# Kernel tuning notes

Measured on AMD Instinct MI355X. Metric: run time of the kernel, lower is better.

Reference implementation:

```python
import jax, jax.numpy as jnp
import numpy as np

NEG_INF = -1e9
NEG_SLOPE = 0.2


def setup_inputs() -> dict:
    key = jax.random.key(0)
    k1, k2, k3, k4, k5 = jax.random.split(key, 5)
    N, in_dim, out_dim = 8192, 256, 128
    x = jax.random.normal(k1, (N, in_dim), dtype=jnp.float32)
    adj = jax.random.randint(k2, (N, N), 0, 2, dtype=jnp.int32)
    # xavier_uniform for W (stored as [in_dim, out_dim] so h = x @ W)
    limit = float(np.sqrt(6.0 / (in_dim + out_dim)))
    W = jax.random.uniform(k3, (in_dim, out_dim), minval=-limit, maxval=limit, dtype=jnp.float32)
    a_src = 0.1 * jax.random.normal(k4, (out_dim,), dtype=jnp.float32)
    a_dst = 0.1 * jax.random.normal(k5, (out_dim,), dtype=jnp.float32)
    return {"x": x, "adj": adj, "W": W, "a_src": a_src, "a_dst": a_dst}


def reference(x, adj, W, a_src, a_dst):
    # h: [N, out_dim]
    h = x @ W
    src = h @ a_src  # [N]
    dst = h @ a_dst  # [N]
    e = jax.nn.leaky_relu(src[:, None] + dst[None, :], negative_slope=NEG_SLOPE)
    e = jnp.where(adj > 0, e, NEG_INF)
    alpha = jax.nn.softmax(e, axis=1)  # row-wise softmax over neighbors
    # dropout is identity in eval mode (reference uses training=False)
    return alpha @ h
```

## Files before the change

### kernel.cpp

```cpp
#include <hip/hip_runtime.h>
#include <hip/hip_bf16.h>

typedef __attribute__((ext_vector_type(8))) short bf16x8;
typedef __attribute__((ext_vector_type(4))) float f32x4;
typedef __attribute__((ext_vector_type(16))) float f32x16;

#define N_NODES 8192
#define D_IN    256
#define D_OUT   128
#define LOG2E   1.44269504088896f

__device__ __forceinline__ unsigned short bf16_rne(float f) {
  unsigned int u = __float_as_uint(f);
  u += 0x7fffu + ((u >> 16) & 1u);
  return (unsigned short)(u >> 16);
}
__device__ __forceinline__ float bf16_to_f(unsigned short s) {
  return __uint_as_float(((unsigned int)s) << 16);
}
__device__ __forceinline__ unsigned int pack_bf16x2(float lo, float hi) {
  __hip_bfloat162 b2 = __float22bfloat162_rn(make_float2(lo, hi));
  union { __hip_bfloat162 b; unsigned int u; } cv;
  cv.b = b2;
  return cv.u;
}

__global__ __launch_bounds__(256) void k_split_w(const float* __restrict__ W,
                                                 unsigned short* __restrict__ whiT,
                                                 unsigned short* __restrict__ wloT) {
  int c = blockIdx.x;
  int k = threadIdx.x;
  float v = W[k * D_OUT + c];
  unsigned short h = bf16_rne(v);
  unsigned short l = bf16_rne(v - bf16_to_f(h));
  whiT[c * D_IN + k] = h;
  wloT[c * D_IN + k] = l;
}

__global__ __launch_bounds__(256) void k_h_gemm(const float* __restrict__ x,
                                                const unsigned short* __restrict__ whiT,
                                                const unsigned short* __restrict__ wloT,
                                                const float* __restrict__ a_src,
                                                const float* __restrict__ a_dst,
                                                float* __restrict__ srcv,
                                                float* __restrict__ dstv,
                                                unsigned short* __restrict__ phi) {
  __shared__ float h_s[32][128];
  const int t = threadIdx.x, l = t & 63, wv = t >> 6;
  const int i0 = blockIdx.x * 32;
  const int m = wv >> 1, nh = wv & 1;
  const int frow = l & 15, kq = l >> 4;
  const size_t arow = (size_t)(i0 + m * 16 + frow);
  const float* px = x + arow * D_IN + kq * 8;
  f32x4 acc[4];
#pragma unroll
  for (int nf = 0; nf < 4; ++nf) acc[nf] = (f32x4){0.f, 0.f, 0.f, 0.f};
#pragma unroll
  for (int kk = 0; kk < 8; ++kk) {
    const int k0 = kk * 32;
    float4 xv0 = *(const float4*)(px + k0);
    float4 xv1 = *(const float4*)(px + k0 + 4);
    float xv[8] = {xv0.x, xv0.y, xv0.z, xv0.w, xv1.x, xv1.y, xv1.z, xv1.w};
    union { bf16x8 v; unsigned short s[8]; } ah, al;
#pragma unroll
    for (int e = 0; e < 8; ++e) {
      ah.s[e] = bf16_rne(xv[e]);
      al.s[e] = bf16_rne(xv[e] - bf16_to_f(ah.s[e]));
    }
#pragma unroll
    for (int nf = 0; nf < 4; ++nf) {
      const int col = nh * 64 + nf * 16 + frow;
      bf16x8 bh = *(const bf16x8*)(whiT + (size_t)col * D_IN + k0 + kq * 8);
      bf16x8 bl = *(const bf16x8*)(wloT + (size_t)col * D_IN + k0 + kq * 8);
      acc[nf] = __builtin_amdgcn_mfma_f32_16x16x32_bf16(ah.v, bh, acc[nf], 0, 0, 0);
      acc[nf] = __builtin_amdgcn_mfma_f32_16x16x32_bf16(al.v, bh, acc[nf], 0, 0, 0);
      acc[nf] = __builtin_amdgcn_mfma_f32_16x16x32_bf16(ah.v, bl, acc[nf], 0, 0, 0);
    }
  }
#pragma unroll
  for (int nf = 0; nf < 4; ++nf)
#pragma unroll
    for (int r = 0; r < 4; ++r)
      h_s[m * 16 + kq * 4 + r][nh * 64 + nf * 16 + frow] = acc[nf][r];
  __syncthreads();

  if (t < 32) {
    float s = 0.f, d = 0.f;
#pragma unroll
    for (int c = 0; c < D_OUT; ++c) {
      float v = h_s[t][c];
      s += v * a_src[c];
      d += v * a_dst[c];
    }
    srcv[i0 + t] = s * LOG2E;
    dstv[i0 + t] = d * LOG2E;
  }

  {
    const int b = t >> 7, ct = (t >> 5) & 3, lw = t & 31;
    const size_t kg = (size_t)(i0 / 16 + b);
#pragma unroll
    for (int half = 0; half < 2; ++half) {
      const int lane = lw + 32 * half;
      unsigned int hw[4];
#pragma unroll
      for (int p = 0; p < 4; ++p) {
        float v0 = h_s[b * 16 + half * 8 + 2 * p][ct * 32 + lw];
        float v1 = h_s[b * 16 + half * 8 + 2 * p + 1][ct * 32 + lw];
        hw[p] = (unsigned int)bf16_rne(v0) | ((unsigned int)bf16_rne(v1) << 16);
      }
      const size_t off = ((kg * 4 + ct) * 64 + lane) * 8;
      *(uint4*)(phi + off) = make_uint4(hw[0], hw[1], hw[2], hw[3]);
    }
  }
}

__global__ __launch_bounds__(512) __attribute__((amdgpu_waves_per_eu(4, 4)))
void k_gat(const int* __restrict__ adj,
           const float* __restrict__ srcv,
           const float* __restrict__ dstv,
           const unsigned short* __restrict__ phi,
           float* __restrict__ pnum,
           float* __restrict__ prsum) {
  __shared__ unsigned long long mbuf[2][4][33];
  __shared__ float dstv_s[4096];
  __shared__ float red[2][2048];
  __shared__ float rsl[4][32];

  const int t = threadIdx.x, l = t & 63, wv = t >> 6;
  const int ch = wv >> 2, js = wv & 3;
  const int bid = blockIdx.x;
  const int tile = bid & 255, jh = bid >> 8;
  const int i0 = tile * 32;
  const int r32 = l & 31, kh = l >> 5;

  ((float4*)dstv_s)[t] = ((const float4*)(dstv + jh * 4096))[t];
  ((float4*)dstv_s)[t + 512] = ((const float4*)(dstv + jh * 4096))[t + 512];
  const float s2 = srcv[i0 + r32];

  const int* abase = adj + (size_t)(i0 + 4 * wv) * N_NODES + jh * 4096 + l;

  int cva[16];
#pragma unroll
  for (int s = 0; s < 16; ++s)
    cva[s] = __builtin_nontemporal_load(abase + (s >> 2) * N_NODES + (s & 3) * 64);
#pragma unroll
  for (int s = 0; s < 16; ++s) {
    unsigned long long b = __ballot(cva[s] > 0);
    if (l == 0) mbuf[0][s & 3][4 * wv + (s >> 2)] = b;
  }
#pragma unroll
  for (int s = 0; s < 16; ++s)
    cva[s] = __builtin_nontemporal_load(abase + (s >> 2) * N_NODES + 256 + (s & 3) * 64);

  const int kst0 = jh * 256 + js * 2;
  const unsigned short* pb0 = phi + ((size_t)(kst0 * 4 + ch * 2) * 64 + l) * 8;
  bf16x8 b00A = *(const bf16x8*)(pb0);
  bf16x8 b01A = *(const bf16x8*)(pb0 + 512);
  bf16x8 b10A = *(const bf16x8*)(pb0 + 2048);
  bf16x8 b11A = *(const bf16x8*)(pb0 + 2048 + 512);

  const int shl = (js & 1) * 32 + kh * 8;
  const int w0 = js >> 1;

  f32x16 acc0, acc1;
#pragma unroll
  for (int q = 0; q < 16; ++q) { acc0[q] = 0.f; acc1[q] = 0.f; }
  float rs = 0.f;

  __syncthreads();

  for (int c = 0; c < 16; ++c) {
#pragma unroll
    for (int it = 0; it < 2; ++it) {
      int nc = c, nit = it + 1;
      if (nit == 2) { nit = 0; nc = (c < 15) ? c + 1 : 15; }
      const unsigned short* pan = pb0 + nc * 32768 + nit * 16384;
      bf16x8 b00B = *(const bf16x8*)(pan);
      bf16x8 b01B = *(const bf16x8*)(pan + 512);
      bf16x8 b10B = *(const bf16x8*)(pan + 2048);
      bf16x8 b11B = *(const bf16x8*)(pan + 2048 + 512);
      __builtin_amdgcn_sched_barrier(0);

      const unsigned long long mw = mbuf[c & 1][it * 2 + w0][r32];
      const int jl = c * 256 + it * 128 + js * 32 + kh * 8;
      const unsigned int u0 = (unsigned int)(mw >> shl) & 0xFFu;
      const unsigned int u1 = (unsigned int)(mw >> (shl + 16)) & 0xFFu;

#pragma unroll
      for (int ks = 0; ks < 2; ++ks) {
        f32x4 dva = *(const f32x4*)&dstv_s[jl + ks * 16];
        f32x4 dvb = *(const f32x4*)&dstv_s[jl + ks * 16 + 4];
        const unsigned int u = ks ? u1 : u0;
        float w[8];
#pragma unroll
        for (int e = 0; e < 4; ++e) {
          float e0 = s2 + dva[e]; e0 = fmaxf(e0, 0.2f * e0);
          float e1 = s2 + dvb[e]; e1 = fmaxf(e1, 0.2f * e1);
          w[e]     = ((u >> e) & 1u)       ? __builtin_amdgcn_exp2f(e0) : 0.f;
          w[4 + e] = ((u >> (4 + e)) & 1u) ? __builtin_amdgcn_exp2f(e1) : 0.f;
        }
        if (ch == 0)
          rs += ((w[0] + w[1]) + (w[2] + w[3])) + ((w[4] + w[5]) + (w[6] + w[7]));
        union { bf16x8 v; unsigned int u4[4]; } af;
#pragma unroll
        for (int p = 0; p < 4; ++p)
          af.u4[p] = pack_bf16x2(w[2 * p], w[2 * p + 1]);

        if (ks == 0) {
          acc0 = __builtin_amdgcn_mfma_f32_32x32x16_bf16(af.v, b00A, acc0, 0, 0, 0);
          acc1 = __builtin_amdgcn_mfma_f32_32x32x16_bf16(af.v, b01A, acc1, 0, 0, 0);
        } else {
          acc0 = __builtin_amdgcn_mfma_f32_32x32x16_bf16(af.v, b10A, acc0, 0, 0, 0);
          acc1 = __builtin_amdgcn_mfma_f32_32x32x16_bf16(af.v, b11A, acc1, 0, 0, 0);
        }
      }
      b00A = b00B; b01A = b01B; b10A = b10B; b11A = b11B;
    }

    if (c < 15) {
#pragma unroll
      for (int s = 0; s < 16; ++s) {
        unsigned long long b = __ballot(cva[s] > 0);
        if (l == 0) mbuf[(c + 1) & 1][s & 3][4 * wv + (s >> 2)] = b;
      }
      if (c < 14) {
        const int nb = (c + 2) * 256;
#pragma unroll
        for (int s = 0; s < 16; ++s)
          cva[s] = __builtin_nontemporal_load(abase + (s >> 2) * N_NODES + nb + (s & 3) * 64);
      }
    }
    __syncthreads();
  }

  rs += __shfl_xor(rs, 32);
  if (ch == 0 && kh == 0) rsl[js][r32] = rs;

#pragma unroll
  for (int q = 1; q < 4; ++q) {
    if (js == q) {
#pragma unroll
      for (int reg = 0; reg < 16; ++reg) {
        red[ch][reg * 64 + l] = acc0[reg];
        red[ch][1024 + reg * 64 + l] = acc1[reg];
      }
    }
    __syncthreads();
    if (js == 0) {
#pragma unroll
      for (int reg = 0; reg < 16; ++reg) {
        acc0[reg] += red[ch][reg * 64 + l];
        acc1[reg] += red[ch][1024 + reg * 64 + l];
      }
    }
    __syncthreads();
  }

  if (js == 0) {
    float* pn = pnum + (size_t)bid * 4096;
#pragma unroll
    for (int reg = 0; reg < 16; ++reg) {
      const int row = (reg & 3) + 8 * (reg >> 2) + 4 * kh;
      pn[row * 128 + ch * 64 + r32] = acc0[reg];
      pn[row * 128 + ch * 64 + 32 + r32] = acc1[reg];
    }
    if (ch == 0 && kh == 0)
      prsum[bid * 32 + r32] = (rsl[0][r32] + rsl[1][r32]) + (rsl[2][r32] + rsl[3][r32]);
  }
}

__global__ __launch_bounds__(1024) void k_comb(const float* __restrict__ pnum,
                                               const float* __restrict__ prsum,
                                               float* __restrict__ out) {
  const int tile = blockIdx.x, t = threadIdx.x;
  const float4 a = ((const float4*)(pnum + (size_t)tile * 4096))[t];
  const float4 b = ((const float4*)(pnum + (size_t)(256 + tile) * 4096))[t];
  const int row = t >> 5;
  const float r = prsum[tile * 32 + row] + prsum[(256 + tile) * 32 + row];
  float4 o;
  o.x = (a.x + b.x) / r;
  o.y = (a.y + b.y) / r;
  o.z = (a.z + b.z) / r;
  o.w = (a.w + b.w) / r;
  ((float4*)(out + (size_t)tile * 4096))[t] = o;
}

extern "C" void kernel_launch(void* const* d_in, const int* in_sizes, int n_in,
                              void* d_out, int out_size, void* d_ws, size_t ws_size,
                              hipStream_t stream) {
  const float* x     = (const float*)d_in[0];
  const int*   adj   = (const int*)d_in[1];
  const float* W     = (const float*)d_in[2];
  const float* a_src = (const float*)d_in[3];
  const float* a_dst = (const float*)d_in[4];
  float* out = (float*)d_out;

  char* ws = (char*)d_ws;
  float*          pnum = (float*)(ws);
  float*          prsum= (float*)(ws + (8 << 20));
  unsigned short* whiT = (unsigned short*)(ws + (8 << 20) + (64 << 10));
  unsigned short* wloT = (unsigned short*)(ws + (8 << 20) + (128 << 10));
  unsigned short* phi  = (unsigned short*)(ws + (8 << 20) + (192 << 10));
  float*          srcv = (float*)(ws + (10 << 20) + (192 << 10));
  float*          dstv = (float*)(ws + (10 << 20) + (224 << 10));

  k_split_w<<<dim3(128), dim3(256), 0, stream>>>(W, whiT, wloT);
  k_h_gemm<<<dim3(256), dim3(256), 0, stream>>>(x, whiT, wloT,
                                                a_src, a_dst, srcv, dstv, phi);
  k_gat<<<dim3(512), dim3(512), 0, stream>>>(adj, srcv, dstv, phi, pnum, prsum);
  k_comb<<<dim3(256), dim3(1024), 0, stream>>>(pnum, prsum, out);
}
```

Measured before the change: 99.34 us.

## Give each wave all 128 output columns and split the key range eight ways

Each of the 8 waves now covers all 128 output columns with four accumulators, and the key dimension is split across eight waves instead of four waves times two column halves. The exp/leaky-relu weight computation is no longer duplicated across two column-half waves, which halves the VALU and transcendental work. In exchange the register prefetch of the next B fragments is dropped, loading 8 fragments per chunk synchronously, and the final cross-wave reduction grows to 7 rounds with larger accumulator state. Register pressure rises under the 4-waves-per-EU constraint.

```diff
diff --git a/kernel.cpp b/kernel.cpp
--- a/kernel.cpp
+++ b/kernel.cpp
@@ -124,11 +124,11 @@
            float* __restrict__ prsum) {
   __shared__ unsigned long long mbuf[2][4][33];
   __shared__ float dstv_s[4096];
-  __shared__ float red[2][2048];
-  __shared__ float rsl[4][32];
+  __shared__ float red[4][1024];
+  __shared__ float rsl[8][32];
 
   const int t = threadIdx.x, l = t & 63, wv = t >> 6;
-  const int ch = wv >> 2, js = wv & 3;
+  const int js = wv;
   const int bid = blockIdx.x;
   const int tile = bid & 255, jh = bid >> 8;
   const int i0 = tile * 32;
@@ -154,68 +154,75 @@
     cva[s] = __builtin_nontemporal_load(abase + (s >> 2) * N_NODES + 256 + (s & 3) * 64);
 
   const int kst0 = jh * 256 + js * 2;
-  const unsigned short* pb0 = phi + ((size_t)(kst0 * 4 + ch * 2) * 64 + l) * 8;
-  bf16x8 b00A = *(const bf16x8*)(pb0);
-  bf16x8 b01A = *(const bf16x8*)(pb0 + 512);
-  bf16x8 b10A = *(const bf16x8*)(pb0 + 2048);
-  bf16x8 b11A = *(const bf16x8*)(pb0 + 2048 + 512);
-
+  const unsigned short* pb0 = phi + ((size_t)(kst0 * 4) * 64 + l) * 8;
+
+  const int wrd = js >> 1;
   const int shl = (js & 1) * 32 + kh * 8;
-  const int w0 = js >> 1;
-
-  f32x16 acc0, acc1;
-#pragma unroll
-  for (int q = 0; q < 16; ++q) { acc0[q] = 0.f; acc1[q] = 0.f; }
+
+  f32x16 acc0, acc1, acc2, acc3;
+#pragma unroll
+  for (int q = 0; q < 16; ++q) { acc0[q] = 0.f; acc1[q] = 0.f; acc2[q] = 0.f; acc3[q] = 0.f; }
   float rs = 0.f;
 
   __syncthreads();
 
   for (int c = 0; c < 16; ++c) {
-#pragma unroll
-    for (int it = 0; it < 2; ++it) {
-      int nc = c, nit = it + 1;
-      if (nit == 2) { nit = 0; nc = (c < 15) ? c + 1 : 15; }
-      const unsigned short* pan = pb0 + nc * 32768 + nit * 16384;
-      bf16x8 b00B = *(const bf16x8*)(pan);
-      bf16x8 b01B = *(const bf16x8*)(pan + 512);
-      bf16x8 b10B = *(const bf16x8*)(pan + 2048);
-      bf16x8 b11B = *(const bf16x8*)(pan + 2048 + 512);
-      __builtin_amdgcn_sched_barrier(0);
-
-      const unsigned long long mw = mbuf[c & 1][it * 2 + w0][r32];
-      const int jl = c * 256 + it * 128 + js * 32 + kh * 8;
-      const unsigned int u0 = (unsigned int)(mw >> shl) & 0xFFu;
-      const unsigned int u1 = (unsigned int)(mw >> (shl + 16)) & 0xFFu;
-
-#pragma unroll
-      for (int ks = 0; ks < 2; ++ks) {
-        f32x4 dva = *(const f32x4*)&dstv_s[jl + ks * 16];
-        f32x4 dvb = *(const f32x4*)&dstv_s[jl + ks * 16 + 4];
-        const unsigned int u = ks ? u1 : u0;
-        float w[8];
-#pragma unroll
-        for (int e = 0; e < 4; ++e) {
-          float e0 = s2 + dva[e]; e0 = fmaxf(e0, 0.2f * e0);
-          float e1 = s2 + dvb[e]; e1 = fmaxf(e1, 0.2f * e1);
-          w[e]     = ((u >> e) & 1u)       ? __builtin_amdgcn_exp2f(e0) : 0.f;
-          w[4 + e] = ((u >> (4 + e)) & 1u) ? __builtin_amdgcn_exp2f(e1) : 0.f;
-        }
-        if (ch == 0)
-          rs += ((w[0] + w[1]) + (w[2] + w[3])) + ((w[4] + w[5]) + (w[6] + w[7]));
-        union { bf16x8 v; unsigned int u4[4]; } af;
-#pragma unroll
-        for (int p = 0; p < 4; ++p)
-          af.u4[p] = pack_bf16x2(w[2 * p], w[2 * p + 1]);
-
-        if (ks == 0) {
-          acc0 = __builtin_amdgcn_mfma_f32_32x32x16_bf16(af.v, b00A, acc0, 0, 0, 0);
-          acc1 = __builtin_amdgcn_mfma_f32_32x32x16_bf16(af.v, b01A, acc1, 0, 0, 0);
-        } else {
-          acc0 = __builtin_amdgcn_mfma_f32_32x32x16_bf16(af.v, b10A, acc0, 0, 0, 0);
-          acc1 = __builtin_amdgcn_mfma_f32_32x32x16_bf16(af.v, b11A, acc1, 0, 0, 0);
-        }
-      }
-      b00A = b00B; b01A = b01B; b10A = b10B; b11A = b11B;
+    const unsigned short* pc = pb0 + c * 32768;
+    bf16x8 b0 = *(const bf16x8*)(pc);
+    bf16x8 b1 = *(const bf16x8*)(pc + 512);
+    bf16x8 b2 = *(const bf16x8*)(pc + 1024);
+    bf16x8 b3 = *(const bf16x8*)(pc + 1536);
+    bf16x8 b4 = *(const bf16x8*)(pc + 2048);
+    bf16x8 b5 = *(const bf16x8*)(pc + 2048 + 512);
+    bf16x8 b6 = *(const bf16x8*)(pc + 2048 + 1024);
+    bf16x8 b7 = *(const bf16x8*)(pc + 2048 + 1536);
+
+    const unsigned long long mw = mbuf[c & 1][wrd][r32];
+    const int jl = c * 256 + js * 32 + kh * 8;
+    const unsigned int u0 = (unsigned int)(mw >> shl) & 0xFFu;
+    const unsigned int u1 = (unsigned int)(mw >> (shl + 16)) & 0xFFu;
+
+    {
+      f32x4 dva = *(const f32x4*)&dstv_s[jl];
+      f32x4 dvb = *(const f32x4*)&dstv_s[jl + 4];
+      float w[8];
+#pragma unroll
+      for (int e = 0; e < 4; ++e) {
+        float e0 = s2 + dva[e]; e0 = fmaxf(e0, 0.2f * e0);
+        float e1 = s2 + dvb[e]; e1 = fmaxf(e1, 0.2f * e1);
+        w[e]     = ((u0 >> e) & 1u)       ? __builtin_amdgcn_exp2f(e0) : 0.f;
+        w[4 + e] = ((u0 >> (4 + e)) & 1u) ? __builtin_amdgcn_exp2f(e1) : 0.f;
+      }
+      rs += ((w[0] + w[1]) + (w[2] + w[3])) + ((w[4] + w[5]) + (w[6] + w[7]));
+      union { bf16x8 v; unsigned int u4[4]; } af;
+#pragma unroll
+      for (int p = 0; p < 4; ++p)
+        af.u4[p] = pack_bf16x2(w[2 * p], w[2 * p + 1]);
+      acc0 = __builtin_amdgcn_mfma_f32_32x32x16_bf16(af.v, b0, acc0, 0, 0, 0);
+      acc1 = __builtin_amdgcn_mfma_f32_32x32x16_bf16(af.v, b1, acc1, 0, 0, 0);
+      acc2 = __builtin_amdgcn_mfma_f32_32x32x16_bf16(af.v, b2, acc2, 0, 0, 0);
+      acc3 = __builtin_amdgcn_mfma_f32_32x32x16_bf16(af.v, b3, acc3, 0, 0, 0);
+    }
+    {
+      f32x4 dva = *(const f32x4*)&dstv_s[jl + 16];
+      f32x4 dvb = *(const f32x4*)&dstv_s[jl + 20];
+      float w[8];
+#pragma unroll
+      for (int e = 0; e < 4; ++e) {
+        float e0 = s2 + dva[e]; e0 = fmaxf(e0, 0.2f * e0);
+        float e1 = s2 + dvb[e]; e1 = fmaxf(e1, 0.2f * e1);
+        w[e]     = ((u1 >> e) & 1u)       ? __builtin_amdgcn_exp2f(e0) : 0.f;
+        w[4 + e] = ((u1 >> (4 + e)) & 1u) ? __builtin_amdgcn_exp2f(e1) : 0.f;
+      }
+      rs += ((w[0] + w[1]) + (w[2] + w[3])) + ((w[4] + w[5]) + (w[6] + w[7]));
+      union { bf16x8 v; unsigned int u4[4]; } af;
+#pragma unroll
+      for (int p = 0; p < 4; ++p)
+        af.u4[p] = pack_bf16x2(w[2 * p], w[2 * p + 1]);
+      acc0 = __builtin_amdgcn_mfma_f32_32x32x16_bf16(af.v, b4, acc0, 0, 0, 0);
+      acc1 = __builtin_amdgcn_mfma_f32_32x32x16_bf16(af.v, b5, acc1, 0, 0, 0);
+      acc2 = __builtin_amdgcn_mfma_f32_32x32x16_bf16(af.v, b6, acc2, 0, 0, 0);
+      acc3 = __builtin_amdgcn_mfma_f32_32x32x16_bf16(af.v, b7, acc3, 0, 0, 0);
     }
 
     if (c < 15) {
@@ -235,23 +242,27 @@
   }
 
   rs += __shfl_xor(rs, 32);
-  if (ch == 0 && kh == 0) rsl[js][r32] = rs;
-
-#pragma unroll
-  for (int q = 1; q < 4; ++q) {
+  if (kh == 0) rsl[js][r32] = rs;
+
+#pragma unroll
+  for (int q = 1; q < 8; ++q) {
     if (js == q) {
 #pragma unroll
       for (int reg = 0; reg < 16; ++reg) {
-        red[ch][reg * 64 + l] = acc0[reg];
-        red[ch][1024 + reg * 64 + l] = acc1[reg];
+        red[0][reg * 64 + l] = acc0[reg];
+        red[1][reg * 64 + l] = acc1[reg];
+        red[2][reg * 64 + l] = acc2[reg];
+        red[3][reg * 64 + l] = acc3[reg];
       }
     }
     __syncthreads();
     if (js == 0) {
 #pragma unroll
       for (int reg = 0; reg < 16; ++reg) {
-        acc0[reg] += red[ch][reg * 64 + l];
-        acc1[reg] += red[ch][1024 + reg * 64 + l];
+        acc0[reg] += red[0][reg * 64 + l];
+        acc1[reg] += red[1][reg * 64 + l];
+        acc2[reg] += red[2][reg * 64 + l];
+        acc3[reg] += red[3][reg * 64 + l];
       }
     }
     __syncthreads();
@@ -262,11 +273,14 @@
 #pragma unroll
     for (int reg = 0; reg < 16; ++reg) {
       const int row = (reg & 3) + 8 * (reg >> 2) + 4 * kh;
-      pn[row * 128 + ch * 64 + r32] = acc0[reg];
-      pn[row * 128 + ch * 64 + 32 + r32] = acc1[reg];
-    }
-    if (ch == 0 && kh == 0)
-      prsum[bid * 32 + r32] = (rsl[0][r32] + rsl[1][r32]) + (rsl[2][r32] + rsl[3][r32]);
+      pn[row * 128 + r32]      = acc0[reg];
+      pn[row * 128 + 32 + r32] = acc1[reg];
+      pn[row * 128 + 64 + r32] = acc2[reg];
+      pn[row * 128 + 96 + r32] = acc3[reg];
+    }
+    if (kh == 0)
+      prsum[bid * 32 + r32] = (((rsl[0][r32] + rsl[1][r32]) + (rsl[2][r32] + rsl[3][r32])) +
+                               ((rsl[4][r32] + rsl[5][r32]) + (rsl[6][r32] + rsl[7][r32])));
   }
 }
 
```

New measurement: 208.0 us. 109% more time.
